# Kernel optimization log

Hardware: AMD Instinct MI355X
Metric: run time of the kernel (lower is better)

The kernel has to match this reference:

```python
import jax, jax.numpy as jnp
import numpy as np

B, S = 32, 128          # batch, seq_len
C, K = 256, 128         # num_concept, dim_k (== dim_e == dim_correct)
DC = 128                # dim_correct
NQ, NIT, NUT = 10000, 1024, 1024


def _xavier(k, shape):
    fan_out, fan_in = shape[0], shape[1]
    bound = float(np.sqrt(6.0 / (fan_in + fan_out)))
    return jax.random.uniform(k, shape, jnp.float32, -bound, bound)


def setup_inputs() -> dict:
    key = jax.random.key(0)
    ks = jax.random.split(key, 16)
    question_seq = jax.random.randint(ks[0], (B, S), 0, NQ + 1)
    interval_time_seq = jax.random.randint(ks[1], (B, S), 0, NIT + 1)
    use_time_seq = jax.random.randint(ks[2], (B, S), 0, NUT + 1)
    correct_seq = jnp.round(jax.random.uniform(ks[3], (B, S))).astype(jnp.float32)
    E_q = _xavier(ks[4], (NQ + 1, K))
    E_it = _xavier(ks[5], (NIT + 1, K))
    E_ut = _xavier(ks[6], (NUT + 1, K))
    q_matrix = (jax.random.uniform(ks[7], (NQ + 1, C)) < 0.03).astype(jnp.float32)
    h0 = _xavier(ks[8], (C, K))  # xavier init of the initial concept memory
    W1 = _xavier(ks[9], (K, K + K + DC)); b1 = jnp.zeros((K,), jnp.float32)
    W2 = _xavier(ks[10], (K, 4 * K));     b2 = jnp.zeros((K,), jnp.float32)
    W3 = _xavier(ks[11], (K, 4 * K));     b3 = jnp.zeros((K,), jnp.float32)
    W4 = _xavier(ks[12], (K, 3 * K));     b4 = jnp.zeros((K,), jnp.float32)
    W5 = _xavier(ks[13], (K, 2 * K));     b5 = jnp.zeros((K,), jnp.float32)
    return dict(question_seq=question_seq, interval_time_seq=interval_time_seq,
                use_time_seq=use_time_seq, correct_seq=correct_seq,
                E_q=E_q, E_it=E_it, E_ut=E_ut, q_matrix=q_matrix, h0=h0,
                W1=W1, b1=b1, W2=W2, b2=b2, W3=W3, b3=b3,
                W4=W4, b4=b4, W5=W5, b5=b5)


def _forward(question_seq, interval_time_seq, use_time_seq, correct_seq,
             E_q, E_it, E_ut, q_matrix, h0,
             W1, b1, W2, b2, W3, b3, W4, b4, W5, b5):
    bsz, slen = question_seq.shape
    dim_k = h0.shape[1]
    dim_c = W1.shape[1] - 2 * dim_k

    q_emb = E_q[question_seq]            # [B,S,K]
    it_emb = E_it[interval_time_seq]     # [B,S,K]
    ut_emb = E_ut[use_time_seq]          # [B,S,K]
    c_emb = jnp.broadcast_to(correct_seq[..., None], (bsz, slen, dim_c))
    all_learning = jnp.concatenate([q_emb, ut_emb, c_emb], -1) @ W1.T + b1  # [B,S,K]
    qe = q_matrix[question_seq]          # [B,S,C]

    h_pre0 = jnp.tile(h0[None], (bsz, 1, 1))                     # [B,C,K]
    h_tilde0 = jnp.einsum('bc,bck->bk', qe[:, 0], h_pre0)        # q_e @ h at t=0
    learning0 = jnp.zeros((bsz, dim_k), all_learning.dtype)

    # split linear_4 weight over its (h_pre, LG, it) concat blocks
    W4h, W4l, W4i = W4[:, :dim_k], W4[:, dim_k:2 * dim_k], W4[:, 2 * dim_k:]

    # time-major per-step inputs for t = 0 .. S-2
    xs = (jnp.swapaxes(it_emb[:, :-1], 0, 1),
          jnp.swapaxes(all_learning[:, :-1], 0, 1),
          jnp.swapaxes(qe[:, :-1], 0, 1),
          jnp.swapaxes(qe[:, 1:], 0, 1),
          jnp.swapaxes(q_emb[:, 1:], 0, 1))

    def step(carry, x):
        h_pre, h_tilde_pre, learning_pre = carry
        it, learning, qe_t, qe_n, qemb_n = x
        cat = jnp.concatenate([learning_pre, it, learning, h_tilde_pre], -1)  # [B,4K]
        learning_gain = jnp.tanh(cat @ W2.T + b2)
        gamma_l = jax.nn.sigmoid(cat @ W3.T + b3)
        LG = gamma_l * (learning_gain + 1.0) * 0.5                 # [B,K]
        LG_tilde = qe_t[:, :, None] * LG[:, None, :]               # [B,C,K] outer write
        gamma_f = jax.nn.sigmoid(jnp.einsum('bck,jk->bcj', h_pre, W4h)
                                 + (LG @ W4l.T + it @ W4i.T + b4)[:, None, :])
        h = LG_tilde + gamma_f * h_pre                             # [B,C,K]
        h_tilde = jnp.einsum('bc,bck->bk', qe_n, h)                # read for t+1
        y = jax.nn.sigmoid(jnp.concatenate([qemb_n, h_tilde], -1) @ W5.T + b5).sum(-1) / dim_k
        return (h, h_tilde, learning), y

    _, ys = jax.lax.scan(step, (h_pre0, h_tilde0, learning0), xs)  # ys: [S-1,B]
    pred = jnp.concatenate([jnp.zeros((bsz, 1), ys.dtype), ys.T], axis=1)
    return pred


def reference(question_seq, interval_time_seq, use_time_seq, correct_seq,
              E_q, E_it, E_ut, q_matrix, h0,
              W1, b1, W2, b2, W3, b3, W4, b4, W5, b5):
    return _forward(question_seq, interval_time_seq, use_time_seq, correct_seq,
                    E_q, E_it, E_ut, q_matrix, h0,
                    W1, b1, W2, b2, W3, b3, W4, b4, W5, b5)
```

## Files before the change

### kernel.cpp

```cpp
#include <hip/hip_runtime.h>
#include <hip/hip_bf16.h>


typedef __bf16 bf16x8 __attribute__((ext_vector_type(8)));
typedef __bf16 bf16x4 __attribute__((ext_vector_type(4)));
typedef float f32x4 __attribute__((ext_vector_type(4)));

#define HBIDX(c,k) ((((c)<<7)) + ((k) ^ (((c)&15)<<3)))

__device__ __forceinline__ float sigmf(float x){
  return __builtin_amdgcn_rcpf(1.0f + __expf(-x));
}

__device__ __forceinline__ bf16x8 cvt8(float4 a, float4 b){
  bf16x8 r;
  r[0]=(__bf16)a.x; r[1]=(__bf16)a.y; r[2]=(__bf16)a.z; r[3]=(__bf16)a.w;
  r[4]=(__bf16)b.x; r[5]=(__bf16)b.y; r[6]=(__bf16)b.z; r[7]=(__bf16)b.w;
  return r;
}

__device__ __forceinline__ void mk_hilo(float4 a, float4 b, bf16x8& hi, bf16x8& lo){
  float v[8] = {a.x,a.y,a.z,a.w,b.x,b.y,b.z,b.w};
  #pragma unroll
  for (int i = 0; i < 8; i++){
    __bf16 h = (__bf16)v[i];
    hi[i] = h;
    lo[i] = (__bf16)(v[i] - (float)h);
  }
}

__device__ __forceinline__ f32x4 mfma16(bf16x8 a, bf16x8 b, f32x4 c){
  return __builtin_amdgcn_mfma_f32_16x16x32_bf16(a, b, c, 0, 0, 0);
}

__device__ __forceinline__ void red16(f32x4& r){
  #pragma unroll
  for (int m = 1; m < 16; m <<= 1){
    r[0] += __shfl_xor(r[0], m);
    r[1] += __shfl_xor(r[1], m);
    r[2] += __shfl_xor(r[2], m);
    r[3] += __shfl_xor(r[3], m);
  }
}

__global__ __launch_bounds__(256) void k1_al(
    const int* __restrict__ qseq, const int* __restrict__ utseq,
    const float* __restrict__ corr,
    const float* __restrict__ Eq, const float* __restrict__ Eut,
    const float* __restrict__ W1, const float* __restrict__ b1,
    const float* __restrict__ W5, const float* __restrict__ b5,
    float* __restrict__ AL, float* __restrict__ pre5)
{
  __shared__ __bf16 inA[64*256];
  __shared__ float corrs[64];
  __shared__ float b1s[128], b5s[128], rsp[256];
  const int tid = threadIdx.x, blk = blockIdx.x;
  if (tid < 128){ b1s[tid]=b1[tid]; b5s[tid]=b5[tid]; }
  {
    int j = tid & 127, hf = tid >> 7;
    const float* p = W1 + j*384 + 256 + hf*64;
    float s = 0.f;
    for (int i = 0; i < 64; i++) s += p[i];
    rsp[tid] = s;
  }
  {
    int r = tid >> 2, seg = tid & 3;
    int R = blk*64 + r;
    int qi = qseq[R], ui = utseq[R];
    if (seg == 0) corrs[r] = corr[R];
    for (int i = 0; i < 64; i++){
      int col = seg*64 + i;
      float v = (col < 128) ? Eq[qi*128 + col] : Eut[ui*128 + (col-128)];
      inA[((r*256 + col) ^ ((r&7)<<3))] = (__bf16)v;
    }
  }
  __syncthreads();
  const int w = tid >> 6, lane = tid & 63;
  const int la = lane & 15, g = lane >> 4;
  const int rbase = w*16;
  bf16x8 af[8];
  #pragma unroll
  for (int kt = 0; kt < 8; kt++){
    int idx = ((rbase+la)*256 + kt*32 + g*8) ^ ((la&7)<<3);
    af[kt] = *(const bf16x8*)&inA[idx];
  }
  for (int jt = 0; jt < 8; jt++){
    f32x4 acc = {0.f,0.f,0.f,0.f};
    const float* Wb = W1 + (jt*16+la)*384;
    #pragma unroll
    for (int kt = 0; kt < 8; kt++){
      const float* p = Wb + kt*32 + g*8;
      acc = mfma16(af[kt], cvt8(*(const float4*)p, *(const float4*)(p+4)), acc);
    }
    int j = jt*16 + la;
    float rsj = rsp[j] + rsp[j+128];
    #pragma unroll
    for (int rr = 0; rr < 4; rr++){
      int row = rbase + g*4 + rr;
      int R = blk*64 + row;
      AL[R*128 + j] = acc[rr] + b1s[j] + corrs[row]*rsj;
    }
  }
  for (int jt = 0; jt < 8; jt++){
    f32x4 acc = {0.f,0.f,0.f,0.f};
    const float* Wb = W5 + (jt*16+la)*256;
    #pragma unroll
    for (int kt = 0; kt < 4; kt++){
      const float* p = Wb + kt*32 + g*8;
      acc = mfma16(af[kt], cvt8(*(const float4*)p, *(const float4*)(p+4)), acc);
    }
    int j = jt*16 + la;
    #pragma unroll
    for (int rr = 0; rr < 4; rr++){
      int row = rbase + g*4 + rr;
      int R = blk*64 + row;
      pre5[R*128 + j] = acc[rr] + b5s[j];
    }
  }
}

__global__ __launch_bounds__(256) void k2_pre(
    const int* __restrict__ itseq, const float* __restrict__ Eit,
    const float* __restrict__ AL,
    const float* __restrict__ W2, const float* __restrict__ W3,
    const float* __restrict__ W4,
    const float* __restrict__ b2, const float* __restrict__ b3,
    const float* __restrict__ b4,
    float* __restrict__ pre23, float* __restrict__ pre4)
{
  __shared__ __bf16 inA[64*384];
  __shared__ int obase[64];
  __shared__ float b2s[128], b3s[128], b4s[128];
  const int tid = threadIdx.x, blk = blockIdx.x;
  if (tid < 128){ b2s[tid]=b2[tid]; b3s[tid]=b3[tid]; b4s[tid]=b4[tid]; }
  {
    int r = tid >> 2, seg = tid & 3;
    int R = blk*64 + r;
    bool valid = (R < 4064);
    int b_ = R / 127, tau = R % 127;
    if (seg == 0) obase[r] = valid ? (b_*127 + tau) : -1;
    int itv = valid ? itseq[b_*128 + tau] : 0;
    for (int i = 0; i < 96; i++){
      int col = seg*96 + i;
      float v = 0.f;
      if (valid){
        if (col < 128)      v = (tau > 0) ? AL[(b_*128 + tau-1)*128 + col] : 0.f;
        else if (col < 256) v = Eit[itv*128 + (col-128)];
        else                v = AL[(b_*128 + tau)*128 + (col-256)];
      }
      inA[((r*384 + col) ^ ((r&7)<<3))] = (__bf16)v;
    }
  }
  __syncthreads();
  const int w = tid >> 6, lane = tid & 63;
  const int la = lane & 15, g = lane >> 4;
  const int rbase = w*16;
  bf16x8 af[12];
  #pragma unroll
  for (int kt = 0; kt < 12; kt++){
    int idx = ((rbase+la)*384 + kt*32 + g*8) ^ ((la&7)<<3);
    af[kt] = *(const bf16x8*)&inA[idx];
  }
  for (int jt = 0; jt < 16; jt++){
    f32x4 acc = {0.f,0.f,0.f,0.f};
    int j = jt*16 + la;
    const float* Wb = (j < 128) ? (W2 + j*512) : (W3 + (j-128)*512);
    #pragma unroll
    for (int kt = 0; kt < 12; kt++){
      const float* p = Wb + kt*32 + g*8;
      acc = mfma16(af[kt], cvt8(*(const float4*)p, *(const float4*)(p+4)), acc);
    }
    float bias = (j < 128) ? b2s[j] : b3s[j-128];
    #pragma unroll
    for (int rr = 0; rr < 4; rr++){
      int row = rbase + g*4 + rr;
      int ob = obase[row];
      if (ob >= 0) pre23[ob*256 + j] = acc[rr] + bias;
    }
  }
  for (int jt = 0; jt < 8; jt++){
    f32x4 acc = {0.f,0.f,0.f,0.f};
    int j = jt*16 + la;
    const float* Wb = W4 + j*384 + 256;
    #pragma unroll
    for (int kk = 0; kk < 4; kk++){
      const float* p = Wb + kk*32 + g*8;
      acc = mfma16(af[4+kk], cvt8(*(const float4*)p, *(const float4*)(p+4)), acc);
    }
    #pragma unroll
    for (int rr = 0; rr < 4; rr++){
      int row = rbase + g*4 + rr;
      int ob = obase[row];
      if (ob >= 0) pre4[ob*128 + j] = acc[rr] + b4s[j];
    }
  }
}

#define SCAN_LDS_BYTES (34880*4)

__global__ __launch_bounds__(512, 2) void lpkt_scan(
    const float* __restrict__ qmat, const int* __restrict__ qseq,
    const float* __restrict__ h0,
    const float* __restrict__ W2, const float* __restrict__ W3,
    const float* __restrict__ W4,
    const float* __restrict__ pre23, const float* __restrict__ pre4,
    float* __restrict__ hist)
{
  extern __shared__ float lds[];
  __bf16* hB  = (__bf16*)lds;
  float*  htb0 = lds + 32768;
  float*  htb1 = lds + 32896;
  float*  LGb  = lds + 33024;
  __bf16* LGh  = (__bf16*)(lds + 33152);
  float*  qeb  = lds + 33216;
  float*  p23L = lds + 33984;
  float*  p4L  = lds + 34496;
  int*    qsl  = (int*)(lds + 34752);

  const int tid  = threadIdx.x;
  const int b    = blockIdx.x;
  const int lane = tid & 63;
  const int w    = tid >> 6;
  const int la   = lane & 15, g = lane >> 4;
  const int jq   = w & 3;
  const int ch   = w >> 2;

  bf16x8 af[2][4];
  bf16x8 af4l[2][4];
  #pragma unroll
  for (int jj = 0; jj < 2; jj++){
    #pragma unroll
    for (int kt = 0; kt < 4; kt++){
      const float* ph = W4 + ((jq*2+jj)*16+la)*384 + kt*32 + g*8;
      const float* pl = W4 + ((jq*2+jj)*16+la)*384 + 128 + kt*32 + g*8;
      af[jj][kt]   = cvt8(*(const float4*)ph, *(const float4*)(ph+4));
      af4l[jj][kt] = cvt8(*(const float4*)pl, *(const float4*)(pl+4));
    }
  }
  bf16x8 af23[2][4];
  #pragma unroll
  for (int kt = 0; kt < 4; kt++){
    const float* p2 = W2 + (w*16+la)*512 + 384 + kt*32 + g*8;
    const float* p3 = W3 + (w*16+la)*512 + 384 + kt*32 + g*8;
    af23[0][kt] = cvt8(*(const float4*)p2, *(const float4*)(p2+4));
    af23[1][kt] = cvt8(*(const float4*)p3, *(const float4*)(p3+4));
  }

  if (tid < 128) qsl[tid] = qseq[b*128 + tid];
  __syncthreads();
  const float* pre23b = pre23 + b*127*256;
  const float* pre4b  = pre4  + b*127*128;
  if (tid < 64)       *(float4*)&qeb[tid*4] = *(const float4*)(qmat + (size_t)qsl[0]*256 + tid*4);
  else if (tid < 128) *(float4*)&qeb[256 + (tid-64)*4] = *(const float4*)(qmat + (size_t)qsl[1]*256 + (tid-64)*4);
  else if (tid < 192) *(float4*)&p23L[(tid-128)*4] = *(const float4*)(pre23b + (tid-128)*4);
  else if (tid < 224) *(float4*)&p4L[(tid-192)*4]  = *(const float4*)(pre4b  + (tid-192)*4);
  else if (tid < 256){ float4 z4i = {0.f,0.f,0.f,0.f}; *(float4*)&htb0[(tid-224)*4] = z4i; }

  float4 hreg[8][2];
  #pragma unroll
  for (int cg = 0; cg < 8; cg++){
    const int c_ = ch*128 + cg*16 + la;
    #pragma unroll
    for (int jj = 0; jj < 2; jj++){
      const int k0 = (jq*2+jj)*16 + g*4;
      float4 v = *(const float4*)(h0 + c_*128 + k0);
      hreg[cg][jj] = v;
      bf16x4 hb; hb[0]=(__bf16)v.x; hb[1]=(__bf16)v.y; hb[2]=(__bf16)v.z; hb[3]=(__bf16)v.w;
      *(bf16x4*)&hB[HBIDX(c_, k0)] = hb;
    }
  }
  __syncthreads();
  {
    f32x4 r0 = {0.f,0.f,0.f,0.f}, r1 = {0.f,0.f,0.f,0.f};
    #pragma unroll
    for (int cg = 0; cg < 8; cg++){
      const int c_ = ch*128 + cg*16 + la;
      float q = qeb[c_];
      float4 h0v = hreg[cg][0], h1v = hreg[cg][1];
      r0[0] += q*h0v.x; r0[1] += q*h0v.y; r0[2] += q*h0v.z; r0[3] += q*h0v.w;
      r1[0] += q*h1v.x; r1[1] += q*h1v.y; r1[2] += q*h1v.z; r1[3] += q*h1v.w;
    }
    red16(r0); red16(r1);
    if (la == 0){
      const int k0 = (jq*2)*16 + g*4, k1 = (jq*2+1)*16 + g*4;
      atomicAdd(&htb0[k0+0], r0[0]); atomicAdd(&htb0[k0+1], r0[1]);
      atomicAdd(&htb0[k0+2], r0[2]); atomicAdd(&htb0[k0+3], r0[3]);
      atomicAdd(&htb0[k1+0], r1[0]); atomicAdd(&htb0[k1+1], r1[1]);
      atomicAdd(&htb0[k1+2], r1[2]); atomicAdd(&htb0[k1+3], r1[3]);
    }
  }
  __syncthreads();

  int i0 = 0, i1 = 1, i2 = 2;

  for (int tau = 0; tau < 127; tau++){
    float* htc = (tau & 1) ? htb1 : htb0;
    float* htn = (tau & 1) ? htb0 : htb1;
    float* qec = qeb + i0*256;
    float* qen = qeb + i1*256;
    float* qep = qeb + i2*256;
    const float* p23c = p23L + (tau & 1)*256;
    const float* p4c  = p4L  + (tau & 1)*128;
    const __bf16* hBr = hB + (tau & 1)*32768;
    __bf16*       hBw = hB + ((tau+1) & 1)*32768;

    if (tid < 128) htn[tid] = 0.f;
    {
      bf16x8 xh[4], xl[4];
      #pragma unroll
      for (int kt = 0; kt < 4; kt++){
        int k0 = kt*32 + g*8;
        mk_hilo(*(const float4*)&htc[k0], *(const float4*)&htc[k0+4], xh[kt], xl[kt]);
      }
      f32x4 aLh = {0.f,0.f,0.f,0.f}, aLl = {0.f,0.f,0.f,0.f};
      f32x4 aGh = {0.f,0.f,0.f,0.f}, aGl = {0.f,0.f,0.f,0.f};
      #pragma unroll
      for (int kt = 0; kt < 4; kt++){
        aLh = mfma16(af23[0][kt], xh[kt], aLh);
        aLl = mfma16(af23[0][kt], xl[kt], aLl);
        aGh = mfma16(af23[1][kt], xh[kt], aGh);
        aGl = mfma16(af23[1][kt], xl[kt], aGl);
      }
      float4 lp4 = *(const float4*)&p23c[w*16 + g*4];
      float4 gp4 = *(const float4*)&p23c[128 + w*16 + g*4];
      float4 LG4;
      LG4.x = sigmf(aGh[0]+aGl[0]+gp4.x) * sigmf(2.f*(aLh[0]+aLl[0]+lp4.x));
      LG4.y = sigmf(aGh[1]+aGl[1]+gp4.y) * sigmf(2.f*(aLh[1]+aLl[1]+lp4.y));
      LG4.z = sigmf(aGh[2]+aGl[2]+gp4.z) * sigmf(2.f*(aLh[2]+aLl[2]+lp4.z));
      LG4.w = sigmf(aGh[3]+aGl[3]+gp4.w) * sigmf(2.f*(aLh[3]+aLl[3]+lp4.w));
      if (la == 0){
        *(float4*)&LGb[w*16 + g*4] = LG4;
        bf16x4 lgp;
        lgp[0]=(__bf16)LG4.x; lgp[1]=(__bf16)LG4.y;
        lgp[2]=(__bf16)LG4.z; lgp[3]=(__bf16)LG4.w;
        *(bf16x4*)&LGh[w*16 + g*4] = lgp;
      }
    }
    __syncthreads();

    float4 pf23, pf4, pfqe;
    const bool dopf = (tau < 126);
    const bool do23 = dopf && (tid < 64);
    const bool do4  = dopf && (tid >= 64) && (tid < 96);
    const bool doqe = dopf && (tid >= 448);
    if (do23) pf23 = *(const float4*)(pre23b + (tau+1)*256 + tid*4);
    if (do4)  pf4  = *(const float4*)(pre4b  + (tau+1)*128 + (tid-64)*4);
    if (doqe) pfqe = *(const float4*)(qmat + (size_t)qsl[tau+2]*256 + (tid-448)*4);

    float4 z4[2];
    {
      bf16x8 lh[4];
      #pragma unroll
      for (int kt = 0; kt < 4; kt++)
        lh[kt] = *(const bf16x8*)&LGh[kt*32 + g*8];
      #pragma unroll
      for (int jj = 0; jj < 2; jj++){
        f32x4 az = {0.f,0.f,0.f,0.f};
        #pragma unroll
        for (int kt = 0; kt < 4; kt++)
          az = mfma16(af4l[jj][kt], lh[kt], az);
        float4 zp = *(const float4*)&p4c[(jq*2+jj)*16 + g*4];
        z4[jj].x = az[0]+zp.x; z4[jj].y = az[1]+zp.y;
        z4[jj].z = az[2]+zp.z; z4[jj].w = az[3]+zp.w;
      }
    }
    float4 lg4[2];
    #pragma unroll
    for (int jj = 0; jj < 2; jj++)
      lg4[jj] = *(const float4*)&LGb[(jq*2+jj)*16 + g*4];

    f32x4 r0 = {0.f,0.f,0.f,0.f}, r1 = {0.f,0.f,0.f,0.f};
    #pragma unroll
    for (int cg = 0; cg < 8; cg++){
      const int c_ = ch*128 + cg*16 + la;
      bf16x8 bfv[4];
      #pragma unroll
      for (int kt = 0; kt < 4; kt++)
        bfv[kt] = *(const bf16x8*)&hBr[HBIDX(c_, kt*32 + g*8)];
      const float qe_t = qec[c_], qe_n = qen[c_];
      #pragma unroll
      for (int jj = 0; jj < 2; jj++){
        f32x4 acc = {0.f,0.f,0.f,0.f};
        #pragma unroll
        for (int kt = 0; kt < 4; kt++)
          acc = mfma16(af[jj][kt], bfv[kt], acc);
        const int k0 = (jq*2+jj)*16 + g*4;
        float4 hp = hreg[cg][jj];
        float4 hn;
        hn.x = qe_t*lg4[jj].x + sigmf(acc[0] + z4[jj].x)*hp.x;
        hn.y = qe_t*lg4[jj].y + sigmf(acc[1] + z4[jj].y)*hp.y;
        hn.z = qe_t*lg4[jj].z + sigmf(acc[2] + z4[jj].z)*hp.z;
        hn.w = qe_t*lg4[jj].w + sigmf(acc[3] + z4[jj].w)*hp.w;
        hreg[cg][jj] = hn;
        bf16x4 hb; hb[0]=(__bf16)hn.x; hb[1]=(__bf16)hn.y; hb[2]=(__bf16)hn.z; hb[3]=(__bf16)hn.w;
        *(bf16x4*)&hBw[HBIDX(c_, k0)] = hb;
        f32x4& r = (jj == 0) ? r0 : r1;
        r[0] += qe_n*hn.x; r[1] += qe_n*hn.y;
        r[2] += qe_n*hn.z; r[3] += qe_n*hn.w;
      }
    }
    red16(r0); red16(r1);
    if (la == 0){
      const int k0 = (jq*2)*16 + g*4, k1 = (jq*2+1)*16 + g*4;
      atomicAdd(&htn[k0+0], r0[0]); atomicAdd(&htn[k0+1], r0[1]);
      atomicAdd(&htn[k0+2], r0[2]); atomicAdd(&htn[k0+3], r0[3]);
      atomicAdd(&htn[k1+0], r1[0]); atomicAdd(&htn[k1+1], r1[1]);
      atomicAdd(&htn[k1+2], r1[2]); atomicAdd(&htn[k1+3], r1[3]);
    }
    if (do23) *(float4*)&p23L[((tau+1)&1)*256 + tid*4] = pf23;
    if (do4)  *(float4*)&p4L[((tau+1)&1)*128 + (tid-64)*4] = pf4;
    if (doqe) *(float4*)&qep[(tid-448)*4] = pfqe;
    __syncthreads();

    if (tid < 32){
      float4 v = *(const float4*)&htn[tid*4];
      *(float4*)(hist + ((size_t)b*127 + tau)*128 + tid*4) = v;
    }
    int t_ = i0; i0 = i1; i1 = i2; i2 = t_;
  }
}

__global__ __launch_bounds__(128) void k4_y(
    const float* __restrict__ hist, const float* __restrict__ pre5,
    const float* __restrict__ W5, float* __restrict__ out)
{
  const int R = blockIdx.x;
  const int s = R & 127, b = R >> 7;
  const int j = threadIdx.x;
  __shared__ float xs[128];
  __shared__ float partial[2];
  if (s == 0){ if (j == 0) out[R] = 0.f; return; }
  xs[j] = hist[((size_t)b*127 + (s-1))*128 + j];
  __syncthreads();
  const float* wr = W5 + j*256 + 128;
  float acc = pre5[(size_t)R*128 + j];
  #pragma unroll
  for (int k = 0; k < 128; k += 4){
    float4 wv = *(const float4*)&wr[k];
    float4 xv = *(const float4*)&xs[k];
    acc += wv.x*xv.x + wv.y*xv.y + wv.z*xv.z + wv.w*xv.w;
  }
  float v = sigmf(acc);
  #pragma unroll
  for (int m = 1; m < 64; m <<= 1) v += __shfl_xor(v, m);
  if ((j & 63) == 0) partial[j >> 6] = v;
  __syncthreads();
  if (j == 0) out[R] = (partial[0] + partial[1]) * (1.f/128.f);
}

extern "C" void kernel_launch(void* const* d_in, const int* in_sizes, int n_in,
                              void* d_out, int out_size, void* d_ws, size_t ws_size,
                              hipStream_t stream) {
  const int*   qseq  = (const int*)  d_in[0];
  const int*   itseq = (const int*)  d_in[1];
  const int*   utseq = (const int*)  d_in[2];
  const float* corr  = (const float*)d_in[3];
  const float* Eq    = (const float*)d_in[4];
  const float* Eit   = (const float*)d_in[5];
  const float* Eut   = (const float*)d_in[6];
  const float* qmat  = (const float*)d_in[7];
  const float* h0    = (const float*)d_in[8];
  const float* W1    = (const float*)d_in[9];
  const float* b1    = (const float*)d_in[10];
  const float* W2    = (const float*)d_in[11];
  const float* b2    = (const float*)d_in[12];
  const float* W3    = (const float*)d_in[13];
  const float* b3    = (const float*)d_in[14];
  const float* W4    = (const float*)d_in[15];
  const float* b4    = (const float*)d_in[16];
  const float* W5    = (const float*)d_in[17];
  const float* b5    = (const float*)d_in[18];
  float* out = (float*)d_out;

  float* ws    = (float*)d_ws;
  float* AL    = ws;
  float* hist  = ws;
  float* pre5  = ws + 524288;
  float* pre23 = ws + 1048576;
  float* pre4  = ws + 2088960;

  (void)hipFuncSetAttribute(reinterpret_cast<const void*>(&lpkt_scan),
                            hipFuncAttributeMaxDynamicSharedMemorySize,
                            SCAN_LDS_BYTES);

  hipLaunchKernelGGL(k1_al, dim3(64), dim3(256), 0, stream,
                     qseq, utseq, corr, Eq, Eut, W1, b1, W5, b5, AL, pre5);
  hipLaunchKernelGGL(k2_pre, dim3(64), dim3(256), 0, stream,
                     itseq, Eit, AL, W2, W3, W4, b2, b3, b4, pre23, pre4);
  hipLaunchKernelGGL(lpkt_scan, dim3(32), dim3(512), SCAN_LDS_BYTES, stream,
                     qmat, qseq, h0, W2, W3, W4, pre23, pre4, hist);
  hipLaunchKernelGGL(k4_y, dim3(4096), dim3(128), 0, stream,
                     hist, pre5, W5, out);
}
```

Measured before the change: 904.1 us.

## Pad LDS hidden-state rows, replace atomics with per-half partials, prefetch h tiles

Replaces the XOR-swizzled bf16 hidden-state layout in LDS with padded rows (136 elements) and precomputed per-thread read/write offsets. The LDS float atomicAdds for the h_tilde reduction become plain float4 stores into two partial buffers, one per concept half, which are summed when read. The clearing of htn each step goes away, and the hist write is moved to the next step and to a different thread group. It also double-buffers the hB fragment loads across concept groups so the loads overlap the MFMAs. This costs more LDS space and registers, which could pressure occupancy at two blocks per CU.

```diff
diff --git a/kernel.cpp b/kernel.cpp
--- a/kernel.cpp
+++ b/kernel.cpp
@@ -6,7 +6,8 @@
 typedef __bf16 bf16x4 __attribute__((ext_vector_type(4)));
 typedef float f32x4 __attribute__((ext_vector_type(4)));
 
-#define HBIDX(c,k) ((((c)<<7)) + ((k) ^ (((c)&15)<<3)))
+#define HROW 136
+#define HBUF (256*HROW)
 
 __device__ __forceinline__ float sigmf(float x){
   return __builtin_amdgcn_rcpf(1.0f + __expf(-x));
@@ -196,7 +197,7 @@
   }
 }
 
-#define SCAN_LDS_BYTES (34880*4)
+#define SCAN_LDS_BYTES (37184*4)
 
 __global__ __launch_bounds__(512, 2) void lpkt_scan(
     const float* __restrict__ qmat, const int* __restrict__ qseq,
@@ -207,15 +208,15 @@
     float* __restrict__ hist)
 {
   extern __shared__ float lds[];
-  __bf16* hB  = (__bf16*)lds;
-  float*  htb0 = lds + 32768;
-  float*  htb1 = lds + 32896;
-  float*  LGb  = lds + 33024;
-  __bf16* LGh  = (__bf16*)(lds + 33152);
-  float*  qeb  = lds + 33216;
-  float*  p23L = lds + 33984;
-  float*  p4L  = lds + 34496;
-  int*    qsl  = (int*)(lds + 34752);
+  __bf16* hB   = (__bf16*)lds;
+  float*  htb0 = lds + 34816;
+  float*  htb1 = lds + 35072;
+  float*  LGb  = lds + 35328;
+  __bf16* LGh  = (__bf16*)(lds + 35456);
+  float*  qeb  = lds + 35520;
+  float*  p23L = lds + 36288;
+  float*  p4L  = lds + 36800;
+  int*    qsl  = (int*)(lds + 37056);
 
   const int tid  = threadIdx.x;
   const int b    = blockIdx.x;
@@ -246,6 +247,14 @@
     af23[1][kt] = cvt8(*(const float4*)p3, *(const float4*)(p3+4));
   }
 
+  int rb[8], wb[8];
+  #pragma unroll
+  for (int cg = 0; cg < 8; cg++){
+    const int c_ = ch*128 + cg*16 + la;
+    rb[cg] = c_*HROW + g*8;
+    wb[cg] = c_*HROW + jq*32 + g*4;
+  }
+
   if (tid < 128) qsl[tid] = qseq[b*128 + tid];
   __syncthreads();
   const float* pre23b = pre23 + b*127*256;
@@ -254,7 +263,6 @@
   else if (tid < 128) *(float4*)&qeb[256 + (tid-64)*4] = *(const float4*)(qmat + (size_t)qsl[1]*256 + (tid-64)*4);
   else if (tid < 192) *(float4*)&p23L[(tid-128)*4] = *(const float4*)(pre23b + (tid-128)*4);
   else if (tid < 224) *(float4*)&p4L[(tid-192)*4]  = *(const float4*)(pre4b  + (tid-192)*4);
-  else if (tid < 256){ float4 z4i = {0.f,0.f,0.f,0.f}; *(float4*)&htb0[(tid-224)*4] = z4i; }
 
   float4 hreg[8][2];
   #pragma unroll
@@ -266,7 +274,7 @@
       float4 v = *(const float4*)(h0 + c_*128 + k0);
       hreg[cg][jj] = v;
       bf16x4 hb; hb[0]=(__bf16)v.x; hb[1]=(__bf16)v.y; hb[2]=(__bf16)v.z; hb[3]=(__bf16)v.w;
-      *(bf16x4*)&hB[HBIDX(c_, k0)] = hb;
+      *(bf16x4*)&hB[wb[cg] + jj*16] = hb;
     }
   }
   __syncthreads();
@@ -282,11 +290,10 @@
     }
     red16(r0); red16(r1);
     if (la == 0){
-      const int k0 = (jq*2)*16 + g*4, k1 = (jq*2+1)*16 + g*4;
-      atomicAdd(&htb0[k0+0], r0[0]); atomicAdd(&htb0[k0+1], r0[1]);
-      atomicAdd(&htb0[k0+2], r0[2]); atomicAdd(&htb0[k0+3], r0[3]);
-      atomicAdd(&htb0[k1+0], r1[0]); atomicAdd(&htb0[k1+1], r1[1]);
-      atomicAdd(&htb0[k1+2], r1[2]); atomicAdd(&htb0[k1+3], r1[3]);
+      float4 s0 = {r0[0],r0[1],r0[2],r0[3]};
+      float4 s1 = {r1[0],r1[1],r1[2],r1[3]};
+      *(float4*)&htb0[ch*128 + jq*32 + g*4]      = s0;
+      *(float4*)&htb0[ch*128 + jq*32 + 16 + g*4] = s1;
     }
   }
   __syncthreads();
@@ -301,16 +308,21 @@
     float* qep = qeb + i2*256;
     const float* p23c = p23L + (tau & 1)*256;
     const float* p4c  = p4L  + (tau & 1)*128;
-    const __bf16* hBr = hB + (tau & 1)*32768;
-    __bf16*       hBw = hB + ((tau+1) & 1)*32768;
-
-    if (tid < 128) htn[tid] = 0.f;
+    const int roff = (tau & 1) ? HBUF : 0;
+    const int woff = (tau & 1) ? 0 : HBUF;
+
     {
       bf16x8 xh[4], xl[4];
       #pragma unroll
       for (int kt = 0; kt < 4; kt++){
         int k0 = kt*32 + g*8;
-        mk_hilo(*(const float4*)&htc[k0], *(const float4*)&htc[k0+4], xh[kt], xl[kt]);
+        float4 a0 = *(const float4*)&htc[k0];
+        float4 a1 = *(const float4*)&htc[k0+4];
+        float4 b0 = *(const float4*)&htc[128 + k0];
+        float4 b1v = *(const float4*)&htc[128 + k0+4];
+        a0.x += b0.x; a0.y += b0.y; a0.z += b0.z; a0.w += b0.w;
+        a1.x += b1v.x; a1.y += b1v.y; a1.z += b1v.z; a1.w += b1v.w;
+        mk_hilo(a0, a1, xh[kt], xl[kt]);
       }
       f32x4 aLh = {0.f,0.f,0.f,0.f}, aLl = {0.f,0.f,0.f,0.f};
       f32x4 aGh = {0.f,0.f,0.f,0.f}, aGl = {0.f,0.f,0.f,0.f};
@@ -346,6 +358,13 @@
     if (do23) pf23 = *(const float4*)(pre23b + (tau+1)*256 + tid*4);
     if (do4)  pf4  = *(const float4*)(pre4b  + (tau+1)*128 + (tid-64)*4);
     if (doqe) pfqe = *(const float4*)(qmat + (size_t)qsl[tau+2]*256 + (tid-448)*4);
+    if (tau > 0 && tid >= 96 && tid < 128){
+      int i = (tid - 96)*4;
+      float4 v0 = *(const float4*)&htc[i];
+      float4 v1 = *(const float4*)&htc[128 + i];
+      float4 v = {v0.x+v1.x, v0.y+v1.y, v0.z+v1.z, v0.w+v1.w};
+      *(float4*)(hist + ((size_t)b*127 + (tau-1))*128 + i) = v;
+    }
 
     float4 z4[2];
     {
@@ -369,22 +388,31 @@
     for (int jj = 0; jj < 2; jj++)
       lg4[jj] = *(const float4*)&LGb[(jq*2+jj)*16 + g*4];
 
+    bf16x8 bA[4], bB[4];
+    {
+      const int base = rb[0] + roff;
+      #pragma unroll
+      for (int kt = 0; kt < 4; kt++) bA[kt] = *(const bf16x8*)&hB[base + kt*32];
+    }
     f32x4 r0 = {0.f,0.f,0.f,0.f}, r1 = {0.f,0.f,0.f,0.f};
     #pragma unroll
     for (int cg = 0; cg < 8; cg++){
+      const bf16x8* cur = (cg & 1) ? bB : bA;
+      bf16x8*       nxt = (cg & 1) ? bA : bB;
+      if (cg < 7){
+        const int base = rb[cg+1] + roff;
+        #pragma unroll
+        for (int kt = 0; kt < 4; kt++) nxt[kt] = *(const bf16x8*)&hB[base + kt*32];
+      }
       const int c_ = ch*128 + cg*16 + la;
-      bf16x8 bfv[4];
-      #pragma unroll
-      for (int kt = 0; kt < 4; kt++)
-        bfv[kt] = *(const bf16x8*)&hBr[HBIDX(c_, kt*32 + g*8)];
       const float qe_t = qec[c_], qe_n = qen[c_];
+      const int wbase = wb[cg] + woff;
       #pragma unroll
       for (int jj = 0; jj < 2; jj++){
         f32x4 acc = {0.f,0.f,0.f,0.f};
         #pragma unroll
         for (int kt = 0; kt < 4; kt++)
-          acc = mfma16(af[jj][kt], bfv[kt], acc);
-        const int k0 = (jq*2+jj)*16 + g*4;
+          acc = mfma16(af[jj][kt], cur[kt], acc);
         float4 hp = hreg[cg][jj];
         float4 hn;
         hn.x = qe_t*lg4[jj].x + sigmf(acc[0] + z4[jj].x)*hp.x;
@@ -393,7 +421,7 @@
         hn.w = qe_t*lg4[jj].w + sigmf(acc[3] + z4[jj].w)*hp.w;
         hreg[cg][jj] = hn;
         bf16x4 hb; hb[0]=(__bf16)hn.x; hb[1]=(__bf16)hn.y; hb[2]=(__bf16)hn.z; hb[3]=(__bf16)hn.w;
-        *(bf16x4*)&hBw[HBIDX(c_, k0)] = hb;
+        *(bf16x4*)&hB[wbase + jj*16] = hb;
         f32x4& r = (jj == 0) ? r0 : r1;
         r[0] += qe_n*hn.x; r[1] += qe_n*hn.y;
         r[2] += qe_n*hn.z; r[3] += qe_n*hn.w;
@@ -401,22 +429,24 @@
     }
     red16(r0); red16(r1);
     if (la == 0){
-      const int k0 = (jq*2)*16 + g*4, k1 = (jq*2+1)*16 + g*4;
-      atomicAdd(&htn[k0+0], r0[0]); atomicAdd(&htn[k0+1], r0[1]);
-      atomicAdd(&htn[k0+2], r0[2]); atomicAdd(&htn[k0+3], r0[3]);
-      atomicAdd(&htn[k1+0], r1[0]); atomicAdd(&htn[k1+1], r1[1]);
-      atomicAdd(&htn[k1+2], r1[2]); atomicAdd(&htn[k1+3], r1[3]);
+      float4 s0 = {r0[0],r0[1],r0[2],r0[3]};
+      float4 s1 = {r1[0],r1[1],r1[2],r1[3]};
+      *(float4*)&htn[ch*128 + jq*32 + g*4]      = s0;
+      *(float4*)&htn[ch*128 + jq*32 + 16 + g*4] = s1;
     }
     if (do23) *(float4*)&p23L[((tau+1)&1)*256 + tid*4] = pf23;
     if (do4)  *(float4*)&p4L[((tau+1)&1)*128 + (tid-64)*4] = pf4;
     if (doqe) *(float4*)&qep[(tid-448)*4] = pfqe;
     __syncthreads();
-
-    if (tid < 32){
-      float4 v = *(const float4*)&htn[tid*4];
-      *(float4*)(hist + ((size_t)b*127 + tau)*128 + tid*4) = v;
-    }
     int t_ = i0; i0 = i1; i1 = i2; i2 = t_;
+  }
+
+  if (tid < 32){
+    int i = tid*4;
+    float4 v0 = *(const float4*)&htb1[i];
+    float4 v1 = *(const float4*)&htb1[128 + i];
+    float4 v = {v0.x+v1.x, v0.y+v1.y, v0.z+v1.z, v0.w+v1.w};
+    *(float4*)(hist + ((size_t)b*127 + 126)*128 + i) = v;
   }
 }
 
```

After: 867.4 us. 1.04x faster.
